# Kernel tuning notes

Hardware: AMD Instinct MI355X
Metric: run time of the kernel (lower is better)

Reference implementation:

```python
import jax, jax.numpy as jnp
import numpy as np
from functools import reduce

# 2x2 beamsplitter gate (1/sqrt(2)) * [[1, i], [i, 1]]
BS_2x2 = (1.0 / np.sqrt(2.0)) * np.array([[1 + 0j, 0 + 1j], [0 + 1j, 1 + 0j]], dtype=np.complex64)


def _kron_phase_diag(a, b):
    """Diagonal vector of kron_i diag([e^{i a_i}, e^{i b_i}]) -> shape (2^n,) complex64.

    Mathematically identical to building the dense Kronecker diagonal matrix
    (as the original tf.linalg.LinearOperatorKronecker(...).to_dense()) and
    right-multiplying by it, since M @ diag(d) == M * d.
    """
    pairs = jnp.stack([jnp.exp(1j * a), jnp.exp(1j * b)], axis=1)  # (n, 2)
    n = pairs.shape[0]
    vec = pairs[0]
    for i in range(1, n):  # static small loop over qubits
        vec = jnp.kron(vec, pairs[i])
    return vec


def _bs_full(n):
    # Dense n-fold Kronecker product of the 2x2 beamsplitter, (2^n, 2^n) complex64
    return reduce(jnp.kron, [jnp.asarray(BS_2x2)] * n)


def setup_inputs() -> dict:
    key = jax.random.key(0)
    kx, ka, kb, kt, kp = jax.random.split(key, 5)
    n = 12
    N = 2 ** n
    batch = 64
    two_pi = 2.0 * np.pi
    return {
        "x": jax.random.normal(kx, (batch, 2, N), dtype=jnp.float32),
        "alphas": jax.random.uniform(ka, (n,), dtype=jnp.float32) * two_pi,
        "betas": jax.random.uniform(kb, (n,), dtype=jnp.float32) * two_pi,
        "thetas": jax.random.uniform(kt, (n,), dtype=jnp.float32) * two_pi,
        "phis": jax.random.uniform(kp, (n,), dtype=jnp.float32) * two_pi,
    }


def reference(x, alphas, betas, thetas, phis):
    n = alphas.shape[0]
    bs = _bs_full(n)                                   # (N, N) complex64
    d_in = _kron_phase_diag(alphas, betas)             # (N,)
    d_theta = _kron_phase_diag(thetas, jnp.zeros_like(thetas))
    d_phi = _kron_phase_diag(phis, jnp.zeros_like(phis))

    out = jax.lax.complex(x[:, 0, :], x[:, 1, :])      # (B, N) complex64
    out = (out * d_in) @ bs                            # input phase shifts + beamsplitter
    out = (out * d_theta) @ bs                         # theta shifts + beamsplitter
    out = out * d_phi                                  # final phi shifts
    return jnp.stack([out.real, out.imag], axis=1)     # (B, 2, N) float32
```

## Files before the change

kernel.cpp:

```cpp
#include <hip/hip_runtime.h>
#include <math.h>

#define NN 4096
#define BLK 512
#define EPT 8
#define EXSZ (NN + (NN >> 5))

__device__ __forceinline__ void cmul(float& ar, float& ai, float br, float bi) {
    float nr = ar * br - ai * bi;
    float ni = ar * bi + ai * br;
    ar = nr; ai = ni;
}

__device__ __forceinline__ void bfly_pair(float* vr, float* vi, int a, int b) {
    float ur = vr[a], ui = vi[a], wr = vr[b], wi = vi[b];
    vr[a] = ur - wi; vi[a] = ui + wr;
    vr[b] = wr - ui; vi[b] = wi + ur;
}

__device__ __forceinline__ void bfly3(float* vr, float* vi) {
    bfly_pair(vr, vi, 0, 1); bfly_pair(vr, vi, 2, 3); bfly_pair(vr, vi, 4, 5); bfly_pair(vr, vi, 6, 7);
    bfly_pair(vr, vi, 0, 2); bfly_pair(vr, vi, 1, 3); bfly_pair(vr, vi, 4, 6); bfly_pair(vr, vi, 5, 7);
    bfly_pair(vr, vi, 0, 4); bfly_pair(vr, vi, 1, 5); bfly_pair(vr, vi, 2, 6); bfly_pair(vr, vi, 3, 7);
}

template<int PC, int PN>
__device__ __forceinline__ void exchange(float2* ex, float* vr, float* vi, int t) {
    const int basec = ((t >> PC) << (PC + 3)) | (t & ((1 << PC) - 1));
    #pragma unroll
    for (int r = 0; r < EPT; ++r) {
        int j = basec + (r << PC);
        ex[j + (j >> 5)] = make_float2(vr[r], vi[r]);
    }
    __syncthreads();
    const int basen = ((t >> PN) << (PN + 3)) | (t & ((1 << PN) - 1));
    #pragma unroll
    for (int r = 0; r < EPT; ++r) {
        int j = basen + (r << PN);
        float2 v = ex[j + (j >> 5)];
        vr[r] = v.x; vi[r] = v.y;
    }
}

__global__ __launch_bounds__(BLK) void qubit_layer_kernel(
    const float* __restrict__ x,
    const float* __restrict__ alphas,
    const float* __restrict__ betas,
    const float* __restrict__ thetas,
    const float* __restrict__ phis,
    float* __restrict__ out)
{
    __shared__ float2 ex0[EXSZ];
    __shared__ float2 ex1[EXSZ];
    __shared__ float2 tbl[6][64];

    const int b = blockIdx.x;
    const int t = threadIdx.x;

    if (t < 384) {
        int part = t >> 6;
        int idx  = t & 63;
        int set  = part >> 1;
        int half = part & 1;
        float a = 0.f;
        #pragma unroll
        for (int m = 0; m < 6; ++m) {
            int q = half ? m : (6 + m);
            int bit = (idx >> (5 - m)) & 1;
            float av, bv;
            if (set == 0)      { av = alphas[q]; bv = betas[q]; }
            else if (set == 1) { av = thetas[q]; bv = 0.f; }
            else               { av = phis[q];   bv = 0.f; }
            a += bit ? bv : av;
        }
        float s, c;
        __sincosf(a, &s, &c);
        float sc = (set >= 1 && half == 0) ? (1.0f / 64.0f) : 1.0f;
        tbl[part][idx] = make_float2(c * sc, s * sc);
    }

    float vr[EPT], vi[EPT];

    const float* xr = x + (size_t)b * 2 * NN;
    const float* xi = xr + NN;
    {
        float4 a0 = ((const float4*)(xr + t * EPT))[0];
        float4 a1 = ((const float4*)(xr + t * EPT))[1];
        float4 c0 = ((const float4*)(xi + t * EPT))[0];
        float4 c1 = ((const float4*)(xi + t * EPT))[1];
        vr[0] = a0.x; vr[1] = a0.y; vr[2] = a0.z; vr[3] = a0.w;
        vr[4] = a1.x; vr[5] = a1.y; vr[6] = a1.z; vr[7] = a1.w;
        vi[0] = c0.x; vi[1] = c0.y; vi[2] = c0.z; vi[3] = c0.w;
        vi[4] = c1.x; vi[5] = c1.y; vi[6] = c1.z; vi[7] = c1.w;
    }
    __syncthreads();

    {
        float2 eh = tbl[1][t >> 3];
        #pragma unroll
        for (int r = 0; r < EPT; ++r) {
            float2 el = tbl[0][((t & 7) << 3) + r];
            float er = el.x, ei = el.y;
            cmul(er, ei, eh.x, eh.y);
            cmul(vr[r], vi[r], er, ei);
        }
    }

    bfly3(vr, vi);
    exchange<0, 3>(ex0, vr, vi, t); bfly3(vr, vi);
    exchange<3, 6>(ex1, vr, vi, t); bfly3(vr, vi);
    exchange<6, 9>(ex0, vr, vi, t); bfly3(vr, vi);

    {
        float2 el = tbl[2][t & 63];
        #pragma unroll
        for (int r = 0; r < EPT; ++r) {
            float2 eh = tbl[3][(t >> 6) + (r << 3)];
            float er = el.x, ei = el.y;
            cmul(er, ei, eh.x, eh.y);
            cmul(vr[r], vi[r], er, ei);
        }
    }

    exchange<9, 0>(ex1, vr, vi, t); bfly3(vr, vi);
    exchange<0, 3>(ex0, vr, vi, t); bfly3(vr, vi);
    exchange<3, 6>(ex1, vr, vi, t); bfly3(vr, vi);
    exchange<6, 9>(ex0, vr, vi, t); bfly3(vr, vi);

    float* outr = out + (size_t)b * 2 * NN;
    float* outi = outr + NN;
    {
        float2 el = tbl[4][t & 63];
        #pragma unroll
        for (int r = 0; r < EPT; ++r) {
            float2 eh = tbl[5][(t >> 6) + (r << 3)];
            float er = el.x, ei = el.y;
            cmul(er, ei, eh.x, eh.y);
            cmul(vr[r], vi[r], er, ei);
            outr[t + (r << 9)] = vr[r];
            outi[t + (r << 9)] = vi[r];
        }
    }
}

extern "C" void kernel_launch(void* const* d_in, const int* in_sizes, int n_in,
                              void* d_out, int out_size, void* d_ws, size_t ws_size,
                              hipStream_t stream) {
    const float* x      = (const float*)d_in[0];
    const float* alphas = (const float*)d_in[1];
    const float* betas  = (const float*)d_in[2];
    const float* thetas = (const float*)d_in[3];
    const float* phis   = (const float*)d_in[4];
    float* out = (float*)d_out;

    const int batch = in_sizes[0] / (2 * NN);
    qubit_layer_kernel<<<batch, BLK, 0, stream>>>(x, alphas, betas, thetas, phis, out);
}
```

Baseline: 10.69 us.

## Split qubit layer into two 6-qubit kernels using wave shuffles and workspace transpose

Every gate is a tensor product of per-qubit operations, so the full operator factors into a low-6-qubit part and a high-6-qubit part. The single kernel with 64 blocks becomes two kernels with 512 blocks each. Each kernel applies its six-qubit chain with wavefront xor shuffles instead of LDS exchanges and barriers, and recomputes the phases per lane. An intermediate transposed array in workspace carries data between the two passes. This spreads work over many more CUs, but adds a second launch and an extra global write and read of the state; the old kernel remains as a fallback when workspace is too small.

Measured after the change: 13.53 us. 1.27x slower.

```diff
diff --git a/kernel.cpp b/kernel.cpp
--- a/kernel.cpp
+++ b/kernel.cpp
@@ -2,9 +2,7 @@
 #include <math.h>
 
 #define NN 4096
-#define BLK 512
-#define EPT 8
-#define EXSZ (NN + (NN >> 5))
+#define BATCH 64
 
 __device__ __forceinline__ void cmul(float& ar, float& ai, float br, float bi) {
     float nr = ar * br - ai * bi;
@@ -12,56 +10,132 @@
     ar = nr; ai = ni;
 }
 
+__device__ __forceinline__ void stage(float& re, float& im, int mask) {
+    float pr = __shfl_xor(re, mask);
+    float pi = __shfl_xor(im, mask);
+    re = re - pi;
+    im = im + pr;
+}
+
+__device__ __forceinline__ void chain6(float& re, float& im, float a_th, float a_ph) {
+    #pragma unroll
+    for (int m = 0; m < 6; ++m) stage(re, im, 1 << m);
+    float s, c;
+    __sincosf(a_th, &s, &c);
+    cmul(re, im, c * 0.125f, s * 0.125f);
+    #pragma unroll
+    for (int m = 0; m < 6; ++m) stage(re, im, 1 << m);
+    __sincosf(a_ph, &s, &c);
+    cmul(re, im, c * 0.125f, s * 0.125f);
+}
+
+__global__ __launch_bounds__(512) void kA(
+    const float* __restrict__ x,
+    const float* __restrict__ al, const float* __restrict__ be,
+    const float* __restrict__ th, const float* __restrict__ ph,
+    float2* __restrict__ Z)
+{
+    __shared__ float tre[8][68], tim[8][68];
+    const int t = threadIdx.x;
+    const int w = t >> 6;
+    const int l = t & 63;
+    const int b  = blockIdx.x >> 3;
+    const int h0 = (blockIdx.x & 7) * 8;
+    const int h  = h0 + w;
+
+    float re = x[(size_t)b * 2 * NN + h * 64 + l];
+    float im = x[(size_t)b * 2 * NN + NN + h * 64 + l];
+
+    float a_in = 0.f, a_th = 0.f, a_ph = 0.f;
+    #pragma unroll
+    for (int m = 0; m < 6; ++m) {
+        int bit = (l >> (5 - m)) & 1;
+        int q = 6 + m;
+        a_in += bit ? be[q] : al[q];
+        if (!bit) { a_th += th[q]; a_ph += ph[q]; }
+    }
+    float s, c;
+    __sincosf(a_in, &s, &c);
+    cmul(re, im, c, s);
+    chain6(re, im, a_th, a_ph);
+
+    tre[w][l] = re; tim[w][l] = im;
+    __syncthreads();
+    const int l2 = t >> 3, dh = t & 7;
+    float2 v = make_float2(tre[dh][l2], tim[dh][l2]);
+    Z[(size_t)b * NN + l2 * 64 + h0 + dh] = v;
+}
+
+__global__ __launch_bounds__(512) void kB(
+    const float2* __restrict__ Z,
+    const float* __restrict__ al, const float* __restrict__ be,
+    const float* __restrict__ th, const float* __restrict__ ph,
+    float* __restrict__ out)
+{
+    __shared__ float tre[64][9], tim[64][9];
+    const int t = threadIdx.x;
+    const int w = t >> 6;
+    const int lane = t & 63;
+    const int b  = blockIdx.x >> 3;
+    const int l0 = (blockIdx.x & 7) * 8;
+
+    float2 v = Z[(size_t)b * NN + (l0 + w) * 64 + lane];
+    float re = v.x, im = v.y;
+
+    float a_in = 0.f, a_th = 0.f, a_ph = 0.f;
+    #pragma unroll
+    for (int q = 0; q < 6; ++q) {
+        int bit = (lane >> (5 - q)) & 1;
+        a_in += bit ? be[q] : al[q];
+        if (!bit) { a_th += th[q]; a_ph += ph[q]; }
+    }
+    float s, c;
+    __sincosf(a_in, &s, &c);
+    cmul(re, im, c, s);
+    chain6(re, im, a_th, a_ph);
+
+    tre[lane][w] = re; tim[lane][w] = im;
+    __syncthreads();
+    const int h = t >> 3, dl = t & 7;
+    out[(size_t)b * 2 * NN + h * 64 + l0 + dl]      = tre[h][dl];
+    out[(size_t)b * 2 * NN + NN + h * 64 + l0 + dl] = tim[h][dl];
+}
+
+#define BLK 512
+#define EPT 8
+#define EXSZ (NN + (NN >> 5))
+
 __device__ __forceinline__ void bfly_pair(float* vr, float* vi, int a, int b) {
     float ur = vr[a], ui = vi[a], wr = vr[b], wi = vi[b];
     vr[a] = ur - wi; vi[a] = ui + wr;
     vr[b] = wr - ui; vi[b] = wi + ur;
 }
-
 __device__ __forceinline__ void bfly3(float* vr, float* vi) {
     bfly_pair(vr, vi, 0, 1); bfly_pair(vr, vi, 2, 3); bfly_pair(vr, vi, 4, 5); bfly_pair(vr, vi, 6, 7);
     bfly_pair(vr, vi, 0, 2); bfly_pair(vr, vi, 1, 3); bfly_pair(vr, vi, 4, 6); bfly_pair(vr, vi, 5, 7);
     bfly_pair(vr, vi, 0, 4); bfly_pair(vr, vi, 1, 5); bfly_pair(vr, vi, 2, 6); bfly_pair(vr, vi, 3, 7);
 }
-
 template<int PC, int PN>
 __device__ __forceinline__ void exchange(float2* ex, float* vr, float* vi, int t) {
     const int basec = ((t >> PC) << (PC + 3)) | (t & ((1 << PC) - 1));
     #pragma unroll
-    for (int r = 0; r < EPT; ++r) {
-        int j = basec + (r << PC);
-        ex[j + (j >> 5)] = make_float2(vr[r], vi[r]);
-    }
+    for (int r = 0; r < EPT; ++r) { int j = basec + (r << PC); ex[j + (j >> 5)] = make_float2(vr[r], vi[r]); }
     __syncthreads();
     const int basen = ((t >> PN) << (PN + 3)) | (t & ((1 << PN) - 1));
     #pragma unroll
-    for (int r = 0; r < EPT; ++r) {
-        int j = basen + (r << PN);
-        float2 v = ex[j + (j >> 5)];
-        vr[r] = v.x; vi[r] = v.y;
-    }
-}
-
-__global__ __launch_bounds__(BLK) void qubit_layer_kernel(
-    const float* __restrict__ x,
-    const float* __restrict__ alphas,
-    const float* __restrict__ betas,
-    const float* __restrict__ thetas,
-    const float* __restrict__ phis,
-    float* __restrict__ out)
+    for (int r = 0; r < EPT; ++r) { int j = basen + (r << PN); float2 v = ex[j + (j >> 5)]; vr[r] = v.x; vi[r] = v.y; }
+}
+__global__ __launch_bounds__(BLK) void qubit_layer_fb(
+    const float* __restrict__ x, const float* __restrict__ alphas, const float* __restrict__ betas,
+    const float* __restrict__ thetas, const float* __restrict__ phis, float* __restrict__ out)
 {
     __shared__ float2 ex0[EXSZ];
     __shared__ float2 ex1[EXSZ];
     __shared__ float2 tbl[6][64];
-
     const int b = blockIdx.x;
     const int t = threadIdx.x;
-
     if (t < 384) {
-        int part = t >> 6;
-        int idx  = t & 63;
-        int set  = part >> 1;
-        int half = part & 1;
+        int part = t >> 6, idx = t & 63, set = part >> 1, half = part & 1;
         float a = 0.f;
         #pragma unroll
         for (int m = 0; m < 6; ++m) {
@@ -73,14 +147,11 @@
             else               { av = phis[q];   bv = 0.f; }
             a += bit ? bv : av;
         }
-        float s, c;
-        __sincosf(a, &s, &c);
+        float s, c; __sincosf(a, &s, &c);
         float sc = (set >= 1 && half == 0) ? (1.0f / 64.0f) : 1.0f;
         tbl[part][idx] = make_float2(c * sc, s * sc);
     }
-
     float vr[EPT], vi[EPT];
-
     const float* xr = x + (size_t)b * 2 * NN;
     const float* xi = xr + NN;
     {
@@ -88,13 +159,10 @@
         float4 a1 = ((const float4*)(xr + t * EPT))[1];
         float4 c0 = ((const float4*)(xi + t * EPT))[0];
         float4 c1 = ((const float4*)(xi + t * EPT))[1];
-        vr[0] = a0.x; vr[1] = a0.y; vr[2] = a0.z; vr[3] = a0.w;
-        vr[4] = a1.x; vr[5] = a1.y; vr[6] = a1.z; vr[7] = a1.w;
-        vi[0] = c0.x; vi[1] = c0.y; vi[2] = c0.z; vi[3] = c0.w;
-        vi[4] = c1.x; vi[5] = c1.y; vi[6] = c1.z; vi[7] = c1.w;
-    }
-    __syncthreads();
-
+        vr[0]=a0.x; vr[1]=a0.y; vr[2]=a0.z; vr[3]=a0.w; vr[4]=a1.x; vr[5]=a1.y; vr[6]=a1.z; vr[7]=a1.w;
+        vi[0]=c0.x; vi[1]=c0.y; vi[2]=c0.z; vi[3]=c0.w; vi[4]=c1.x; vi[5]=c1.y; vi[6]=c1.z; vi[7]=c1.w;
+    }
+    __syncthreads();
     {
         float2 eh = tbl[1][t >> 3];
         #pragma unroll
@@ -105,12 +173,10 @@
             cmul(vr[r], vi[r], er, ei);
         }
     }
-
     bfly3(vr, vi);
     exchange<0, 3>(ex0, vr, vi, t); bfly3(vr, vi);
     exchange<3, 6>(ex1, vr, vi, t); bfly3(vr, vi);
     exchange<6, 9>(ex0, vr, vi, t); bfly3(vr, vi);
-
     {
         float2 el = tbl[2][t & 63];
         #pragma unroll
@@ -121,12 +187,10 @@
             cmul(vr[r], vi[r], er, ei);
         }
     }
-
     exchange<9, 0>(ex1, vr, vi, t); bfly3(vr, vi);
     exchange<0, 3>(ex0, vr, vi, t); bfly3(vr, vi);
     exchange<3, 6>(ex1, vr, vi, t); bfly3(vr, vi);
     exchange<6, 9>(ex0, vr, vi, t); bfly3(vr, vi);
-
     float* outr = out + (size_t)b * 2 * NN;
     float* outi = outr + NN;
     {
@@ -152,7 +216,14 @@
     const float* thetas = (const float*)d_in[3];
     const float* phis   = (const float*)d_in[4];
     float* out = (float*)d_out;
-
     const int batch = in_sizes[0] / (2 * NN);
-    qubit_layer_kernel<<<batch, BLK, 0, stream>>>(x, alphas, betas, thetas, phis, out);
-}
+
+    const size_t zbytes = (size_t)batch * NN * sizeof(float2);
+    if (ws_size >= zbytes) {
+        float2* Z = (float2*)d_ws;
+        kA<<<batch * 8, 512, 0, stream>>>(x, alphas, betas, thetas, phis, Z);
+        kB<<<batch * 8, 512, 0, stream>>>(Z, alphas, betas, thetas, phis, out);
+    } else {
+        qubit_layer_fb<<<batch, BLK, 0, stream>>>(x, alphas, betas, thetas, phis, out);
+    }
+}
```

## Drop phase tables, use intra-wave LDS exchanges and reorder second butterfly pass

Applied to the files above, without the earlier changes.

Replaces the shared-memory phase lookup tables with per-element sincos computed from per-thread partial angle sums. This removes the table-build phase and its barrier. The butterfly stages whose data movement stays inside one 64-lane wavefront now skip __syncthreads, and the second pass runs its stages in reverse order so one exchange disappears; only two block barriers remain. Output becomes vectorized float4 stores. The cost is more transcendental math per element, and correctness now depends on wave64 lockstep execution with only a compiler memory fence between LDS write and read.

After: 15.37 us. +43.8%, slower.

```diff
diff --git a/kernel.cpp b/kernel.cpp
--- a/kernel.cpp
+++ b/kernel.cpp
@@ -4,12 +4,15 @@
 #define NN 4096
 #define BLK 512
 #define EPT 8
-#define EXSZ (NN + (NN >> 5))
+#define PADSZ (NN + (NN >> 3))
 
-__device__ __forceinline__ void cmul(float& ar, float& ai, float br, float bi) {
-    float nr = ar * br - ai * bi;
-    float ni = ar * bi + ai * br;
-    ar = nr; ai = ni;
+__device__ __forceinline__ void rot(float& r, float& i, float a, float sc) {
+    float sn, cs;
+    __sincosf(a, &sn, &cs);
+    sn *= sc; cs *= sc;
+    float nr = r * cs - i * sn;
+    float ni = r * sn + i * cs;
+    r = nr; i = ni;
 }
 
 __device__ __forceinline__ void bfly_pair(float* vr, float* vi, int a, int b) {
@@ -24,122 +27,109 @@
     bfly_pair(vr, vi, 0, 4); bfly_pair(vr, vi, 1, 5); bfly_pair(vr, vi, 2, 6); bfly_pair(vr, vi, 3, 7);
 }
 
-template<int PC, int PN>
-__device__ __forceinline__ void exchange(float2* ex, float* vr, float* vi, int t) {
-    const int basec = ((t >> PC) << (PC + 3)) | (t & ((1 << PC) - 1));
+template<int P>
+__device__ __forceinline__ int jidx(int t, int r) {
+    return ((t >> P) << (P + 3)) | (r << P) | (t & ((1 << P) - 1));
+}
+
+template<int PC, int PN, bool CROSS>
+__device__ __forceinline__ void exchange(float2* buf, float* vr, float* vi, int t) {
     #pragma unroll
     for (int r = 0; r < EPT; ++r) {
-        int j = basec + (r << PC);
-        ex[j + (j >> 5)] = make_float2(vr[r], vi[r]);
+        int j = jidx<PC>(t, r);
+        buf[j + (j >> 3)] = make_float2(vr[r], vi[r]);
     }
-    __syncthreads();
-    const int basen = ((t >> PN) << (PN + 3)) | (t & ((1 << PN) - 1));
+    if (CROSS) { __syncthreads(); }
+    else       { asm volatile("" ::: "memory"); }
     #pragma unroll
     for (int r = 0; r < EPT; ++r) {
-        int j = basen + (r << PN);
-        float2 v = ex[j + (j >> 5)];
+        int j = jidx<PN>(t, r);
+        float2 v = buf[j + (j >> 3)];
         vr[r] = v.x; vi[r] = v.y;
     }
 }
 
 __global__ __launch_bounds__(BLK) void qubit_layer_kernel(
     const float* __restrict__ x,
-    const float* __restrict__ alphas,
-    const float* __restrict__ betas,
-    const float* __restrict__ thetas,
-    const float* __restrict__ phis,
+    const float* __restrict__ al, const float* __restrict__ be,
+    const float* __restrict__ th, const float* __restrict__ ph,
     float* __restrict__ out)
 {
-    __shared__ float2 ex0[EXSZ];
-    __shared__ float2 ex1[EXSZ];
-    __shared__ float2 tbl[6][64];
+    __shared__ float2 B1[PADSZ];
+    __shared__ float2 B2[PADSZ];
 
+    const int t = threadIdx.x;
     const int b = blockIdx.x;
-    const int t = threadIdx.x;
-
-    if (t < 384) {
-        int part = t >> 6;
-        int idx  = t & 63;
-        int set  = part >> 1;
-        int half = part & 1;
-        float a = 0.f;
-        #pragma unroll
-        for (int m = 0; m < 6; ++m) {
-            int q = half ? m : (6 + m);
-            int bit = (idx >> (5 - m)) & 1;
-            float av, bv;
-            if (set == 0)      { av = alphas[q]; bv = betas[q]; }
-            else if (set == 1) { av = thetas[q]; bv = 0.f; }
-            else               { av = phis[q];   bv = 0.f; }
-            a += bit ? bv : av;
-        }
-        float s, c;
-        __sincosf(a, &s, &c);
-        float sc = (set >= 1 && half == 0) ? (1.0f / 64.0f) : 1.0f;
-        tbl[part][idx] = make_float2(c * sc, s * sc);
-    }
-
-    float vr[EPT], vi[EPT];
 
     const float* xr = x + (size_t)b * 2 * NN;
     const float* xi = xr + NN;
+    float vr[EPT], vi[EPT];
     {
         float4 a0 = ((const float4*)(xr + t * EPT))[0];
         float4 a1 = ((const float4*)(xr + t * EPT))[1];
         float4 c0 = ((const float4*)(xi + t * EPT))[0];
         float4 c1 = ((const float4*)(xi + t * EPT))[1];
-        vr[0] = a0.x; vr[1] = a0.y; vr[2] = a0.z; vr[3] = a0.w;
-        vr[4] = a1.x; vr[5] = a1.y; vr[6] = a1.z; vr[7] = a1.w;
-        vi[0] = c0.x; vi[1] = c0.y; vi[2] = c0.z; vi[3] = c0.w;
-        vi[4] = c1.x; vi[5] = c1.y; vi[6] = c1.z; vi[7] = c1.w;
+        vr[0]=a0.x; vr[1]=a0.y; vr[2]=a0.z; vr[3]=a0.w; vr[4]=a1.x; vr[5]=a1.y; vr[6]=a1.z; vr[7]=a1.w;
+        vi[0]=c0.x; vi[1]=c0.y; vi[2]=c0.z; vi[3]=c0.w; vi[4]=c1.x; vi[5]=c1.y; vi[6]=c1.z; vi[7]=c1.w;
     }
-    __syncthreads();
 
-    {
-        float2 eh = tbl[1][t >> 3];
-        #pragma unroll
-        for (int r = 0; r < EPT; ++r) {
-            float2 el = tbl[0][((t & 7) << 3) + r];
-            float er = el.x, ei = el.y;
-            cmul(er, ei, eh.x, eh.y);
-            cmul(vr[r], vi[r], er, ei);
-        }
+    float Sin = 0.f, Sth = 0.f, Sph = 0.f;
+    #pragma unroll
+    for (int q = 0; q <= 8; ++q) {
+        int bit = (t >> (8 - q)) & 1;
+        Sin += bit ? be[q] : al[q];
+        Sph += bit ? 0.f : ph[q];
+    }
+    #pragma unroll
+    for (int q = 3; q <= 11; ++q) {
+        int bit = (t >> (11 - q)) & 1;
+        Sth += bit ? 0.f : th[q];
+    }
+
+    #pragma unroll
+    for (int r = 0; r < EPT; ++r) {
+        float a = Sin + (((r >> 2) & 1) ? be[9]  : al[9])
+                      + (((r >> 1) & 1) ? be[10] : al[10])
+                      + ((r & 1)        ? be[11] : al[11]);
+        rot(vr[r], vi[r], a, 1.f);
     }
 
     bfly3(vr, vi);
-    exchange<0, 3>(ex0, vr, vi, t); bfly3(vr, vi);
-    exchange<3, 6>(ex1, vr, vi, t); bfly3(vr, vi);
-    exchange<6, 9>(ex0, vr, vi, t); bfly3(vr, vi);
+    exchange<0, 3, false>(B1, vr, vi, t); bfly3(vr, vi);
+    exchange<3, 6, false>(B1, vr, vi, t); bfly3(vr, vi);
+    exchange<6, 9, true >(B1, vr, vi, t); bfly3(vr, vi);
 
-    {
-        float2 el = tbl[2][t & 63];
-        #pragma unroll
-        for (int r = 0; r < EPT; ++r) {
-            float2 eh = tbl[3][(t >> 6) + (r << 3)];
-            float er = el.x, ei = el.y;
-            cmul(er, ei, eh.x, eh.y);
-            cmul(vr[r], vi[r], er, ei);
-        }
+    #pragma unroll
+    for (int r = 0; r < EPT; ++r) {
+        float a = Sth + (((r >> 2) & 1) ? 0.f : th[0])
+                      + (((r >> 1) & 1) ? 0.f : th[1])
+                      + ((r & 1)        ? 0.f : th[2]);
+        rot(vr[r], vi[r], a, 1.0f / 64.0f);
     }
 
-    exchange<9, 0>(ex1, vr, vi, t); bfly3(vr, vi);
-    exchange<0, 3>(ex0, vr, vi, t); bfly3(vr, vi);
-    exchange<3, 6>(ex1, vr, vi, t); bfly3(vr, vi);
-    exchange<6, 9>(ex0, vr, vi, t); bfly3(vr, vi);
+    bfly3(vr, vi);
+    exchange<9, 6, true >(B2, vr, vi, t); bfly3(vr, vi);
+    exchange<6, 3, false>(B1, vr, vi, t); bfly3(vr, vi);
+    exchange<3, 0, false>(B1, vr, vi, t); bfly3(vr, vi);
 
     float* outr = out + (size_t)b * 2 * NN;
     float* outi = outr + NN;
+    #pragma unroll
+    for (int r = 0; r < EPT; ++r) {
+        float a = Sph + (((r >> 2) & 1) ? 0.f : ph[9])
+                      + (((r >> 1) & 1) ? 0.f : ph[10])
+                      + ((r & 1)        ? 0.f : ph[11]);
+        rot(vr[r], vi[r], a, 1.0f / 64.0f);
+    }
     {
-        float2 el = tbl[4][t & 63];
-        #pragma unroll
-        for (int r = 0; r < EPT; ++r) {
-            float2 eh = tbl[5][(t >> 6) + (r << 3)];
-            float er = el.x, ei = el.y;
-            cmul(er, ei, eh.x, eh.y);
-            cmul(vr[r], vi[r], er, ei);
-            outr[t + (r << 9)] = vr[r];
-            outi[t + (r << 9)] = vi[r];
-        }
+        float4 o0 = make_float4(vr[0], vr[1], vr[2], vr[3]);
+        float4 o1 = make_float4(vr[4], vr[5], vr[6], vr[7]);
+        float4 o2 = make_float4(vi[0], vi[1], vi[2], vi[3]);
+        float4 o3 = make_float4(vi[4], vi[5], vi[6], vi[7]);
+        ((float4*)(outr + t * EPT))[0] = o0;
+        ((float4*)(outr + t * EPT))[1] = o1;
+        ((float4*)(outi + t * EPT))[0] = o2;
+        ((float4*)(outi + t * EPT))[1] = o3;
     }
 }
 
```

## Reverse second butterfly pass and drop intra-wavefront barriers in shared-memory exchanges

Applied to the files above, without the earlier changes.

Exchanges whose data movement stays within a 64-thread wavefront now skip __syncthreads and use only a compiler memory fence, and padding changes to one float2 per 8 entries. The second beamsplitter pass runs its stages in reverse order, so the last exchange returns data to the original contiguous layout. That lets the final phase multiply read float4 table entries and the output be written with vectorized float4 stores. This cuts block-wide barriers and scattered stores, but relies on wavefront-synchronous execution on AMD and on the stage reordering being mathematically equivalent.

Result: faster. 10.26 us (-4.0%).

```diff
diff --git a/kernel.cpp b/kernel.cpp
--- a/kernel.cpp
+++ b/kernel.cpp
@@ -4,7 +4,7 @@
 #define NN 4096
 #define BLK 512
 #define EPT 8
-#define EXSZ (NN + (NN >> 5))
+#define PADSZ (NN + (NN >> 3))
 
 __device__ __forceinline__ void cmul(float& ar, float& ai, float br, float bi) {
     float nr = ar * br - ai * bi;
@@ -24,44 +24,43 @@
     bfly_pair(vr, vi, 0, 4); bfly_pair(vr, vi, 1, 5); bfly_pair(vr, vi, 2, 6); bfly_pair(vr, vi, 3, 7);
 }
 
-template<int PC, int PN>
-__device__ __forceinline__ void exchange(float2* ex, float* vr, float* vi, int t) {
-    const int basec = ((t >> PC) << (PC + 3)) | (t & ((1 << PC) - 1));
+template<int P>
+__device__ __forceinline__ int jidx(int t, int r) {
+    return ((t >> P) << (P + 3)) | (r << P) | (t & ((1 << P) - 1));
+}
+
+template<int PC, int PN, bool CROSS>
+__device__ __forceinline__ void exchange(float2* buf, float* vr, float* vi, int t) {
     #pragma unroll
     for (int r = 0; r < EPT; ++r) {
-        int j = basec + (r << PC);
-        ex[j + (j >> 5)] = make_float2(vr[r], vi[r]);
+        int j = jidx<PC>(t, r);
+        buf[j + (j >> 3)] = make_float2(vr[r], vi[r]);
     }
-    __syncthreads();
-    const int basen = ((t >> PN) << (PN + 3)) | (t & ((1 << PN) - 1));
+    if (CROSS) { __syncthreads(); }
+    else       { asm volatile("" ::: "memory"); }
     #pragma unroll
     for (int r = 0; r < EPT; ++r) {
-        int j = basen + (r << PN);
-        float2 v = ex[j + (j >> 5)];
+        int j = jidx<PN>(t, r);
+        float2 v = buf[j + (j >> 3)];
         vr[r] = v.x; vi[r] = v.y;
     }
 }
 
 __global__ __launch_bounds__(BLK) void qubit_layer_kernel(
     const float* __restrict__ x,
-    const float* __restrict__ alphas,
-    const float* __restrict__ betas,
-    const float* __restrict__ thetas,
-    const float* __restrict__ phis,
+    const float* __restrict__ alphas, const float* __restrict__ betas,
+    const float* __restrict__ thetas, const float* __restrict__ phis,
     float* __restrict__ out)
 {
-    __shared__ float2 ex0[EXSZ];
-    __shared__ float2 ex1[EXSZ];
+    __shared__ float2 B1[PADSZ];
+    __shared__ float2 B2[PADSZ];
     __shared__ float2 tbl[6][64];
 
+    const int t = threadIdx.x;
     const int b = blockIdx.x;
-    const int t = threadIdx.x;
 
     if (t < 384) {
-        int part = t >> 6;
-        int idx  = t & 63;
-        int set  = part >> 1;
-        int half = part & 1;
+        int part = t >> 6, idx = t & 63, set = part >> 1, half = part & 1;
         float a = 0.f;
         #pragma unroll
         for (int m = 0; m < 6; ++m) {
@@ -79,37 +78,37 @@
         tbl[part][idx] = make_float2(c * sc, s * sc);
     }
 
-    float vr[EPT], vi[EPT];
-
     const float* xr = x + (size_t)b * 2 * NN;
     const float* xi = xr + NN;
+    float vr[EPT], vi[EPT];
     {
         float4 a0 = ((const float4*)(xr + t * EPT))[0];
         float4 a1 = ((const float4*)(xr + t * EPT))[1];
         float4 c0 = ((const float4*)(xi + t * EPT))[0];
         float4 c1 = ((const float4*)(xi + t * EPT))[1];
-        vr[0] = a0.x; vr[1] = a0.y; vr[2] = a0.z; vr[3] = a0.w;
-        vr[4] = a1.x; vr[5] = a1.y; vr[6] = a1.z; vr[7] = a1.w;
-        vi[0] = c0.x; vi[1] = c0.y; vi[2] = c0.z; vi[3] = c0.w;
-        vi[4] = c1.x; vi[5] = c1.y; vi[6] = c1.z; vi[7] = c1.w;
+        vr[0]=a0.x; vr[1]=a0.y; vr[2]=a0.z; vr[3]=a0.w; vr[4]=a1.x; vr[5]=a1.y; vr[6]=a1.z; vr[7]=a1.w;
+        vi[0]=c0.x; vi[1]=c0.y; vi[2]=c0.z; vi[3]=c0.w; vi[4]=c1.x; vi[5]=c1.y; vi[6]=c1.z; vi[7]=c1.w;
     }
     __syncthreads();
 
     {
         float2 eh = tbl[1][t >> 3];
+        const float4* elv = (const float4*)&tbl[0][(t & 7) << 3];
         #pragma unroll
-        for (int r = 0; r < EPT; ++r) {
-            float2 el = tbl[0][((t & 7) << 3) + r];
-            float er = el.x, ei = el.y;
-            cmul(er, ei, eh.x, eh.y);
-            cmul(vr[r], vi[r], er, ei);
+        for (int k = 0; k < 4; ++k) {
+            float4 e2 = elv[k];
+            float er0 = e2.x, ei0 = e2.y, er1 = e2.z, ei1 = e2.w;
+            cmul(er0, ei0, eh.x, eh.y);
+            cmul(er1, ei1, eh.x, eh.y);
+            cmul(vr[2*k],   vi[2*k],   er0, ei0);
+            cmul(vr[2*k+1], vi[2*k+1], er1, ei1);
         }
     }
 
     bfly3(vr, vi);
-    exchange<0, 3>(ex0, vr, vi, t); bfly3(vr, vi);
-    exchange<3, 6>(ex1, vr, vi, t); bfly3(vr, vi);
-    exchange<6, 9>(ex0, vr, vi, t); bfly3(vr, vi);
+    exchange<0, 3, false>(B1, vr, vi, t); bfly3(vr, vi);
+    exchange<3, 6, false>(B1, vr, vi, t); bfly3(vr, vi);
+    exchange<6, 9, true >(B1, vr, vi, t); bfly3(vr, vi);
 
     {
         float2 el = tbl[2][t & 63];
@@ -122,24 +121,31 @@
         }
     }
 
-    exchange<9, 0>(ex1, vr, vi, t); bfly3(vr, vi);
-    exchange<0, 3>(ex0, vr, vi, t); bfly3(vr, vi);
-    exchange<3, 6>(ex1, vr, vi, t); bfly3(vr, vi);
-    exchange<6, 9>(ex0, vr, vi, t); bfly3(vr, vi);
+    bfly3(vr, vi);
+    exchange<9, 6, true >(B2, vr, vi, t); bfly3(vr, vi);
+    exchange<6, 3, false>(B1, vr, vi, t); bfly3(vr, vi);
+    exchange<3, 0, false>(B1, vr, vi, t); bfly3(vr, vi);
 
+    {
+        float2 eh = tbl[5][t >> 3];
+        const float4* elv = (const float4*)&tbl[4][(t & 7) << 3];
+        #pragma unroll
+        for (int k = 0; k < 4; ++k) {
+            float4 e2 = elv[k];
+            float er0 = e2.x, ei0 = e2.y, er1 = e2.z, ei1 = e2.w;
+            cmul(er0, ei0, eh.x, eh.y);
+            cmul(er1, ei1, eh.x, eh.y);
+            cmul(vr[2*k],   vi[2*k],   er0, ei0);
+            cmul(vr[2*k+1], vi[2*k+1], er1, ei1);
+        }
+    }
     float* outr = out + (size_t)b * 2 * NN;
     float* outi = outr + NN;
     {
-        float2 el = tbl[4][t & 63];
-        #pragma unroll
-        for (int r = 0; r < EPT; ++r) {
-            float2 eh = tbl[5][(t >> 6) + (r << 3)];
-            float er = el.x, ei = el.y;
-            cmul(er, ei, eh.x, eh.y);
-            cmul(vr[r], vi[r], er, ei);
-            outr[t + (r << 9)] = vr[r];
-            outi[t + (r << 9)] = vi[r];
-        }
+        ((float4*)(outr + t * EPT))[0] = make_float4(vr[0], vr[1], vr[2], vr[3]);
+        ((float4*)(outr + t * EPT))[1] = make_float4(vr[4], vr[5], vr[6], vr[7]);
+        ((float4*)(outi + t * EPT))[0] = make_float4(vi[0], vi[1], vi[2], vi[3]);
+        ((float4*)(outi + t * EPT))[1] = make_float4(vi[4], vi[5], vi[6], vi[7]);
     }
 }
 
```
